# Kernel optimization log

Hardware: AMD Instinct MI355X
Metric: run time of the kernel (lower is better)

The kernel has to match this reference:

```python
import jax, jax.numpy as jnp
import numpy as np
import math

D_MODEL = 1024
N_HEADS = 16
D_HEAD = D_MODEL // N_HEADS
BIAS_HIDDEN = 32
B, N = 2, 1024


def setup_inputs() -> dict:
    key = jax.random.key(0)
    ks = jax.random.split(key, 16)
    s = 1.0 / math.sqrt(D_MODEL)
    inp = {
        "x": jax.random.normal(ks[0], (B, N, D_MODEL), dtype=jnp.float32),
        "xyz": jax.random.normal(ks[1], (B, N, 3), dtype=jnp.float32),
        "Wq": jax.random.normal(ks[2], (D_MODEL, D_MODEL), jnp.float32) * s,
        "bq": jnp.zeros((D_MODEL,), jnp.float32),
        "Wk": jax.random.normal(ks[3], (D_MODEL, D_MODEL), jnp.float32) * s,
        "bk": jnp.zeros((D_MODEL,), jnp.float32),
        "Wv": jax.random.normal(ks[4], (D_MODEL, D_MODEL), jnp.float32) * s,
        "bv": jnp.zeros((D_MODEL,), jnp.float32),
        "Wo": jax.random.normal(ks[5], (D_MODEL, D_MODEL), jnp.float32) * s,
        "bo": jnp.zeros((D_MODEL,), jnp.float32),
        "W1": jax.random.normal(ks[6], (3, BIAS_HIDDEN), jnp.float32) * (1.0 / math.sqrt(3.0)),
        "b1": jnp.zeros((BIAS_HIDDEN,), jnp.float32),
        "W2": jax.random.normal(ks[7], (BIAS_HIDDEN, N_HEADS), jnp.float32) * (1.0 / math.sqrt(BIAS_HIDDEN)),
        "b2": jnp.zeros((N_HEADS,), jnp.float32),
    }
    return inp


def reference(x, xyz, Wq, bq, Wk, bk, Wv, bv, Wo, bo, W1, b1, W2, b2):
    Bv, Nv, _ = x.shape
    # q,k,v projections -> [B, H, N, Dh]
    def proj(W, b):
        return (x @ W + b).reshape(Bv, Nv, N_HEADS, D_HEAD).transpose(0, 2, 1, 3)
    q = proj(Wq, bq)
    k = proj(Wk, bk)
    v = proj(Wv, bv)
    scores = jnp.einsum('bhid,bhjd->bhij', q, k) / math.sqrt(D_HEAD)
    # pairwise relative positions -> per-head bias via tiny MLP
    rel_pos = xyz[:, :, None, :] - xyz[:, None, :, :]            # [B,N,N,3]
    hidden = jax.nn.relu(rel_pos @ W1 + b1)                      # [B,N,N,hid]
    bias = (hidden @ W2 + b2).transpose(0, 3, 1, 2)              # [B,H,N,N]
    attn = jax.nn.softmax(scores + bias, axis=-1)                # [B,H,N,N]
    out = jnp.einsum('bhij,bhjd->bhid', attn, v)                 # [B,H,N,Dh]
    out = out.transpose(0, 2, 1, 3).reshape(Bv, Nv, D_MODEL)
    out = out @ Wo + bo
    return (out, attn)
```

## Files before the change

### kernel.cpp

```cpp
#include <hip/hip_runtime.h>
#include <hip/hip_bf16.h>
#include <math.h>

#define NTOK   1024
#define DMODEL 1024
#define NHEADS 16
#define DHEAD  64

typedef __attribute__((ext_vector_type(8))) short short8;
typedef __attribute__((ext_vector_type(4))) float floatx4;
#define MFMA(a,b,c) __builtin_amdgcn_mfma_f32_16x16x32_bf16(a,b,c,0,0,0)

__device__ __forceinline__ void bf16_split(float f, ushort& h, ushort& l) {
    unsigned u = __float_as_uint(f);
    unsigned hr = (u + 0x7FFFu + ((u >> 16) & 1u)) >> 16;
    h = (ushort)hr;
    float fh = __uint_as_float(hr << 16);
    float res = f - fh;
    unsigned u2 = __float_as_uint(res);
    l = (ushort)((u2 + 0x7FFFu + ((u2 >> 16) & 1u)) >> 16);
}

__global__ __launch_bounds__(256) void bias_kernel(
    const float* __restrict__ xyz,
    const float* __restrict__ W1, const float* __restrict__ b1,
    const float* __restrict__ W2, const float* __restrict__ b2,
    float* __restrict__ attnO)
{
    __shared__ float wbuf[656];
    int tid = threadIdx.x;
    for (int i = tid; i < 656; i += 256) {
        float v;
        if (i < 96)       v = W1[i];
        else if (i < 128) v = b1[i - 96];
        else if (i < 640) v = W2[i - 128];
        else              v = b2[i - 640];
        wbuf[i] = v;
    }
    __syncthreads();
    const float* w1s = wbuf;
    const float* b1s = wbuf + 96;
    const float* w2s = wbuf + 128;
    const float* b2s = wbuf + 640;

    int j = blockIdx.x * 256 + tid;
    int i = blockIdx.y;
    int b = blockIdx.z;

    float xi0 = xyz[((size_t)b * NTOK + i) * 3 + 0];
    float xi1 = xyz[((size_t)b * NTOK + i) * 3 + 1];
    float xi2 = xyz[((size_t)b * NTOK + i) * 3 + 2];
    float d0 = xi0 - xyz[((size_t)b * NTOK + j) * 3 + 0];
    float d1 = xi1 - xyz[((size_t)b * NTOK + j) * 3 + 1];
    float d2 = xi2 - xyz[((size_t)b * NTOK + j) * 3 + 2];

    float h[32];
#pragma unroll
    for (int hh = 0; hh < 32; ++hh) {
        float v = b1s[hh] + d0 * w1s[hh] + d1 * w1s[32 + hh] + d2 * w1s[64 + hh];
        h[hh] = fmaxf(v, 0.f);
    }
    size_t base = (size_t)b * NHEADS * 1048576 + (size_t)i * 1024 + j;
#pragma unroll
    for (int hd = 0; hd < NHEADS; ++hd) {
        float acc = b2s[hd];
#pragma unroll
        for (int hh = 0; hh < 32; ++hh) acc += h[hh] * w2s[hh * 16 + hd];
        attnO[base + (size_t)hd * 1048576] = acc;
    }
}

__global__ __launch_bounds__(256) void convx_kernel(
    const float* __restrict__ x, ushort* __restrict__ xh, ushort* __restrict__ xl)
{
    int id = blockIdx.x * 256 + threadIdx.x;
    float4 v = ((const float4*)x)[id];
    ushort h0,h1,h2,h3,l0,l1,l2,l3;
    bf16_split(v.x,h0,l0); bf16_split(v.y,h1,l1);
    bf16_split(v.z,h2,l2); bf16_split(v.w,h3,l3);
    ushort4 hv; hv.x=h0; hv.y=h1; hv.z=h2; hv.w=h3;
    ushort4 lv; lv.x=l0; lv.y=l1; lv.z=l2; lv.w=l3;
    ((ushort4*)xh)[id] = hv;
    ((ushort4*)xl)[id] = lv;
}

__global__ __launch_bounds__(256) void convw_kernel(
    const float* __restrict__ Wq, const float* __restrict__ Wk,
    const float* __restrict__ Wv, const float* __restrict__ Wo,
    ushort* __restrict__ Wcth, ushort* __restrict__ Wctl,
    ushort* __restrict__ Woth, ushort* __restrict__ Wotl)
{
    __shared__ float t[64][65];
    int z = blockIdx.z;
    const float* W = (z == 0) ? Wq : (z == 1) ? Wk : (z == 2) ? Wv : Wo;
    int n0 = blockIdx.x * 64, k0 = blockIdx.y * 64;
    int tid = threadIdx.x;
    int c4 = tid & 15, rr = tid >> 4;
#pragma unroll
    for (int t4 = 0; t4 < 4; ++t4) {
        int row = rr + t4 * 16;
        float4 v = *(const float4*)&W[(size_t)(k0 + row) * 1024 + n0 + c4 * 4];
        t[row][c4 * 4 + 0] = v.x; t[row][c4 * 4 + 1] = v.y;
        t[row][c4 * 4 + 2] = v.z; t[row][c4 * 4 + 3] = v.w;
    }
    __syncthreads();
    ushort* oh = (z < 3) ? Wcth : Woth;
    ushort* ol = (z < 3) ? Wctl : Wotl;
    int nbase = (z < 3) ? z * 1024 : 0;
#pragma unroll
    for (int t4 = 0; t4 < 4; ++t4) {
        int nl = rr + t4 * 16;
        int kk = c4 * 4;
        ushort4 hv, lv;
        ushort h, l;
        bf16_split(t[kk + 0][nl], h, l); hv.x = h; lv.x = l;
        bf16_split(t[kk + 1][nl], h, l); hv.y = h; lv.y = l;
        bf16_split(t[kk + 2][nl], h, l); hv.z = h; lv.z = l;
        bf16_split(t[kk + 3][nl], h, l); hv.w = h; lv.w = l;
        size_t o = (size_t)(nbase + n0 + nl) * 1024 + k0 + kk;
        *(ushort4*)&oh[o] = hv;
        *(ushort4*)&ol[o] = lv;
    }
}

__global__ __launch_bounds__(256) void mm_kernel(
    const ushort* __restrict__ Ah, const ushort* __restrict__ Al,
    const ushort* __restrict__ Bh, const ushort* __restrict__ Bl,
    const float* __restrict__ bq, const float* __restrict__ bk,
    const float* __restrict__ bv,
    float* __restrict__ out,
    ushort* __restrict__ qh, ushort* __restrict__ ql,
    ushort* __restrict__ kh, ushort* __restrict__ kl,
    ushort* __restrict__ vth, ushort* __restrict__ vtl,
    int mode)
{
    int n0 = blockIdx.x * 64;
    int m0 = blockIdx.y * 128;
    int w = threadIdx.x >> 6, l = threadIdx.x & 63;
    int li = l & 15, lg = l >> 4;
    int mrow = m0 + w * 32;

    const ushort* a0h = Ah + (size_t)(mrow + li) * 1024;
    const ushort* a0l = Al + (size_t)(mrow + li) * 1024;
    const ushort* a1h = Ah + (size_t)(mrow + 16 + li) * 1024;
    const ushort* a1l = Al + (size_t)(mrow + 16 + li) * 1024;
    const ushort* b0h = Bh + (size_t)(n0 +  0 + li) * 1024;
    const ushort* b1h = Bh + (size_t)(n0 + 16 + li) * 1024;
    const ushort* b2h = Bh + (size_t)(n0 + 32 + li) * 1024;
    const ushort* b3h = Bh + (size_t)(n0 + 48 + li) * 1024;
    const ushort* b0l = Bl + (size_t)(n0 +  0 + li) * 1024;
    const ushort* b1l = Bl + (size_t)(n0 + 16 + li) * 1024;
    const ushort* b2l = Bl + (size_t)(n0 + 32 + li) * 1024;
    const ushort* b3l = Bl + (size_t)(n0 + 48 + li) * 1024;

    floatx4 acc[2][4];
#pragma unroll
    for (int i = 0; i < 2; ++i)
#pragma unroll
        for (int j = 0; j < 4; ++j) acc[i][j] = (floatx4){0.f, 0.f, 0.f, 0.f};

    for (int ks = 0; ks < 32; ++ks) {
        int ko = ks * 32 + lg * 8;
        short8 A0h = *(const short8*)(a0h + ko);
        short8 A0l = *(const short8*)(a0l + ko);
        short8 A1h = *(const short8*)(a1h + ko);
        short8 A1l = *(const short8*)(a1l + ko);
#pragma unroll
        for (int nf = 0; nf < 4; ++nf) {
            const ushort* bhp = (nf == 0) ? b0h : (nf == 1) ? b1h : (nf == 2) ? b2h : b3h;
            const ushort* blp = (nf == 0) ? b0l : (nf == 1) ? b1l : (nf == 2) ? b2l : b3l;
            short8 Bh8 = *(const short8*)(bhp + ko);
            short8 Bl8 = *(const short8*)(blp + ko);
            acc[0][nf] = MFMA(A0h, Bh8, acc[0][nf]);
            acc[0][nf] = MFMA(A0h, Bl8, acc[0][nf]);
            acc[0][nf] = MFMA(A0l, Bh8, acc[0][nf]);
            acc[1][nf] = MFMA(A1h, Bh8, acc[1][nf]);
            acc[1][nf] = MFMA(A1h, Bl8, acc[1][nf]);
            acc[1][nf] = MFMA(A1l, Bh8, acc[1][nf]);
        }
    }

    if (mode == 0) {
#pragma unroll
        for (int fm = 0; fm < 2; ++fm)
#pragma unroll
            for (int nf = 0; nf < 4; ++nf) {
                int col = n0 + nf * 16 + li;
                float bval = bq[col];
#pragma unroll
                for (int r = 0; r < 4; ++r) {
                    int row = mrow + fm * 16 + lg * 4 + r;
                    out[(size_t)row * 1024 + col] = acc[fm][nf][r] + bval;
                }
            }
    } else {
        int z = n0 >> 10;
        const float* bp = (z == 0) ? bq : (z == 1) ? bk : bv;
#pragma unroll
        for (int fm = 0; fm < 2; ++fm)
#pragma unroll
            for (int nf = 0; nf < 4; ++nf) {
                int col = n0 + nf * 16 + li;
                int nloc = col & 1023;
                int hd = nloc >> 6, d = nloc & 63;
                float bval = bp[nloc];
#pragma unroll
                for (int r = 0; r < 4; ++r) {
                    int row = mrow + fm * 16 + lg * 4 + r;
                    int b = row >> 10, nn = row & 1023;
                    int bh = b * NHEADS + hd;
                    float v = acc[fm][nf][r] + bval;
                    ushort h, lo; bf16_split(v, h, lo);
                    if (z == 0) {
                        size_t o = ((size_t)bh * NTOK + nn) * DHEAD + d;
                        qh[o] = h; ql[o] = lo;
                    } else if (z == 1) {
                        size_t o = ((size_t)bh * NTOK + nn) * DHEAD + d;
                        kh[o] = h; kl[o] = lo;
                    } else {
                        size_t o = ((size_t)bh * DHEAD + d) * NTOK + nn;
                        vth[o] = h; vtl[o] = lo;
                    }
                }
            }
    }
}

__global__ __launch_bounds__(256) void score_kernel(
    const ushort* __restrict__ qh, const ushort* __restrict__ ql,
    const ushort* __restrict__ kh, const ushort* __restrict__ kl,
    float* __restrict__ attnO)
{
    __shared__ float redM[4][16];
    __shared__ float redS[4][16];
    int qt = blockIdx.x, hd = blockIdx.y, b = blockIdx.z;
    int bh = b * NHEADS + hd;
    int w = threadIdx.x >> 6, l = threadIdx.x & 63;
    int li = l & 15, lg = l >> 4;

    size_t qoff = ((size_t)bh * NTOK + qt * 16 + li) * DHEAD + lg * 8;
    short8 q0h = *(const short8*)(qh + qoff);
    short8 q0l = *(const short8*)(ql + qoff);
    short8 q1h = *(const short8*)(qh + qoff + 32);
    short8 q1l = *(const short8*)(ql + qoff + 32);

    floatx4 acc[16];
#pragma unroll
    for (int jf = 0; jf < 16; ++jf) acc[jf] = (floatx4){0.f, 0.f, 0.f, 0.f};

    int jbase = w * 256;
#pragma unroll
    for (int jf = 0; jf < 16; ++jf) {
        size_t koff = ((size_t)bh * NTOK + jbase + jf * 16 + li) * DHEAD + lg * 8;
        short8 K0h = *(const short8*)(kh + koff);
        short8 K0l = *(const short8*)(kl + koff);
        short8 K1h = *(const short8*)(kh + koff + 32);
        short8 K1l = *(const short8*)(kl + koff + 32);
        acc[jf] = MFMA(q0h, K0h, acc[jf]);
        acc[jf] = MFMA(q0h, K0l, acc[jf]);
        acc[jf] = MFMA(q0l, K0h, acc[jf]);
        acc[jf] = MFMA(q1h, K1h, acc[jf]);
        acc[jf] = MFMA(q1h, K1l, acc[jf]);
        acc[jf] = MFMA(q1l, K1h, acc[jf]);
    }

    float* prow = attnO + ((size_t)bh * NTOK + qt * 16) * NTOK;

    float mloc[4] = {-1e30f, -1e30f, -1e30f, -1e30f};
#pragma unroll
    for (int jf = 0; jf < 16; ++jf)
#pragma unroll
        for (int r = 0; r < 4; ++r) {
            float s = acc[jf][r] * 0.125f
                    + prow[(size_t)(lg * 4 + r) * NTOK + jbase + jf * 16 + li];
            acc[jf][r] = s;
            mloc[r] = fmaxf(mloc[r], s);
        }
#pragma unroll
    for (int r = 0; r < 4; ++r) {
        float m = mloc[r];
        m = fmaxf(m, __shfl_xor(m, 1, 64));
        m = fmaxf(m, __shfl_xor(m, 2, 64));
        m = fmaxf(m, __shfl_xor(m, 4, 64));
        m = fmaxf(m, __shfl_xor(m, 8, 64));
        mloc[r] = m;
    }
    if (li == 0) {
#pragma unroll
        for (int r = 0; r < 4; ++r) redM[w][lg * 4 + r] = mloc[r];
    }
    __syncthreads();
    float M[4];
#pragma unroll
    for (int r = 0; r < 4; ++r) {
        int row = lg * 4 + r;
        M[r] = fmaxf(fmaxf(redM[0][row], redM[1][row]),
                     fmaxf(redM[2][row], redM[3][row]));
    }
    float sloc[4] = {0.f, 0.f, 0.f, 0.f};
#pragma unroll
    for (int jf = 0; jf < 16; ++jf)
#pragma unroll
        for (int r = 0; r < 4; ++r) {
            float e = __expf(acc[jf][r] - M[r]);
            acc[jf][r] = e;
            sloc[r] += e;
        }
#pragma unroll
    for (int r = 0; r < 4; ++r) {
        float s = sloc[r];
        s += __shfl_xor(s, 1, 64);
        s += __shfl_xor(s, 2, 64);
        s += __shfl_xor(s, 4, 64);
        s += __shfl_xor(s, 8, 64);
        sloc[r] = s;
    }
    if (li == 0) {
#pragma unroll
        for (int r = 0; r < 4; ++r) redS[w][lg * 4 + r] = sloc[r];
    }
    __syncthreads();
    float inv[4];
#pragma unroll
    for (int r = 0; r < 4; ++r) {
        int row = lg * 4 + r;
        inv[r] = 1.0f / (redS[0][row] + redS[1][row] + redS[2][row] + redS[3][row]);
    }
#pragma unroll
    for (int jf = 0; jf < 16; ++jf)
#pragma unroll
        for (int r = 0; r < 4; ++r)
            prow[(size_t)(lg * 4 + r) * NTOK + jbase + jf * 16 + li] = acc[jf][r] * inv[r];
}

__global__ __launch_bounds__(256) void pv_kernel(
    const float* __restrict__ attnP,
    const ushort* __restrict__ vth, const ushort* __restrict__ vtl,
    ushort* __restrict__ awh, ushort* __restrict__ awl)
{
    int mt = blockIdx.x;
    int bh = blockIdx.y;
    int b = bh >> 4, hd = bh & 15;
    int w = threadIdx.x >> 6, l = threadIdx.x & 63;
    int li = l & 15, lg = l >> 4;
    int mrow = mt * 128 + w * 32;

    const float* P0 = attnP + ((size_t)bh * NTOK + mrow + li) * NTOK;
    const float* P1 = attnP + ((size_t)bh * NTOK + mrow + 16 + li) * NTOK;
    const ushort* v0h = vth + ((size_t)bh * DHEAD +  0 + li) * NTOK;
    const ushort* v1h = vth + ((size_t)bh * DHEAD + 16 + li) * NTOK;
    const ushort* v2h = vth + ((size_t)bh * DHEAD + 32 + li) * NTOK;
    const ushort* v3h = vth + ((size_t)bh * DHEAD + 48 + li) * NTOK;
    const ushort* v0l = vtl + ((size_t)bh * DHEAD +  0 + li) * NTOK;
    const ushort* v1l = vtl + ((size_t)bh * DHEAD + 16 + li) * NTOK;
    const ushort* v2l = vtl + ((size_t)bh * DHEAD + 32 + li) * NTOK;
    const ushort* v3l = vtl + ((size_t)bh * DHEAD + 48 + li) * NTOK;

    floatx4 acc[2][4];
#pragma unroll
    for (int i = 0; i < 2; ++i)
#pragma unroll
        for (int j = 0; j < 4; ++j) acc[i][j] = (floatx4){0.f, 0.f, 0.f, 0.f};

    for (int ks = 0; ks < 32; ++ks) {
        int ko = ks * 32 + lg * 8;
        float pa[8], pb[8];
        {
            float4 t0 = *(const float4*)(P0 + ko);
            float4 t1 = *(const float4*)(P0 + ko + 4);
            pa[0]=t0.x; pa[1]=t0.y; pa[2]=t0.z; pa[3]=t0.w;
            pa[4]=t1.x; pa[5]=t1.y; pa[6]=t1.z; pa[7]=t1.w;
            float4 t2 = *(const float4*)(P1 + ko);
            float4 t3 = *(const float4*)(P1 + ko + 4);
            pb[0]=t2.x; pb[1]=t2.y; pb[2]=t2.z; pb[3]=t2.w;
            pb[4]=t3.x; pb[5]=t3.y; pb[6]=t3.z; pb[7]=t3.w;
        }
        short8 A0h, A0l, A1h, A1l;
#pragma unroll
        for (int e = 0; e < 8; ++e) {
            ushort h, lo;
            bf16_split(pa[e], h, lo); A0h[e] = (short)h; A0l[e] = (short)lo;
            bf16_split(pb[e], h, lo); A1h[e] = (short)h; A1l[e] = (short)lo;
        }
#pragma unroll
        for (int nf = 0; nf < 4; ++nf) {
            const ushort* vhp = (nf == 0) ? v0h : (nf == 1) ? v1h : (nf == 2) ? v2h : v3h;
            const ushort* vlp = (nf == 0) ? v0l : (nf == 1) ? v1l : (nf == 2) ? v2l : v3l;
            short8 Bh8 = *(const short8*)(vhp + ko);
            short8 Bl8 = *(const short8*)(vlp + ko);
            acc[0][nf] = MFMA(A0h, Bh8, acc[0][nf]);
            acc[0][nf] = MFMA(A0h, Bl8, acc[0][nf]);
            acc[0][nf] = MFMA(A0l, Bh8, acc[0][nf]);
            acc[1][nf] = MFMA(A1h, Bh8, acc[1][nf]);
            acc[1][nf] = MFMA(A1h, Bl8, acc[1][nf]);
            acc[1][nf] = MFMA(A1l, Bh8, acc[1][nf]);
        }
    }
#pragma unroll
    for (int fm = 0; fm < 2; ++fm)
#pragma unroll
        for (int nf = 0; nf < 4; ++nf)
#pragma unroll
            for (int r = 0; r < 4; ++r) {
                int token = mrow + fm * 16 + lg * 4 + r;
                int d = nf * 16 + li;
                float v = acc[fm][nf][r];
                ushort h, lo; bf16_split(v, h, lo);
                size_t o = ((size_t)(b * NTOK + token)) * DMODEL + hd * DHEAD + d;
                awh[o] = h; awl[o] = lo;
            }
}

extern "C" void kernel_launch(void* const* d_in, const int* in_sizes, int n_in,
                              void* d_out, int out_size, void* d_ws, size_t ws_size,
                              hipStream_t stream)
{
    const float* x   = (const float*)d_in[0];
    const float* xyz = (const float*)d_in[1];
    const float* Wq  = (const float*)d_in[2];
    const float* bq  = (const float*)d_in[3];
    const float* Wk  = (const float*)d_in[4];
    const float* bk  = (const float*)d_in[5];
    const float* Wv  = (const float*)d_in[6];
    const float* bv  = (const float*)d_in[7];
    const float* Wo  = (const float*)d_in[8];
    const float* bo  = (const float*)d_in[9];
    const float* W1  = (const float*)d_in[10];
    const float* b1  = (const float*)d_in[11];
    const float* W2  = (const float*)d_in[12];
    const float* b2  = (const float*)d_in[13];

    const size_t OUT_ELEMS = (size_t)2 * NTOK * DMODEL;
    float* out   = (float*)d_out;
    float* attnO = out + OUT_ELEMS;

    char* ws = (char*)d_ws;
    ushort* Wcth = (ushort*)(ws);
    ushort* Wctl = (ushort*)(ws + 6291456);
    ushort* Woth = (ushort*)(ws + 12582912);
    ushort* Wotl = (ushort*)(ws + 14680064);
    ushort* qh   = (ushort*)(ws + 16777216);
    ushort* ql   = (ushort*)(ws + 20971520);
    ushort* kh   = (ushort*)(ws + 25165824);
    ushort* kl   = (ushort*)(ws + 29360128);
    ushort* vth  = (ushort*)(ws + 33554432);
    ushort* vtl  = (ushort*)(ws + 37748736);
    ushort* xh   = (ushort*)(ws + 41943040);
    ushort* xl   = (ushort*)(ws + 46137344);
    ushort* awh  = xh;
    ushort* awl  = xl;

    bias_kernel<<<dim3(4, 1024, 2), 256, 0, stream>>>(xyz, W1, b1, W2, b2, attnO);
    convx_kernel<<<dim3(2048), 256, 0, stream>>>(x, xh, xl);
    convw_kernel<<<dim3(16, 16, 4), 256, 0, stream>>>(Wq, Wk, Wv, Wo,
                                                      Wcth, Wctl, Woth, Wotl);
    mm_kernel<<<dim3(48, 16), 256, 0, stream>>>(xh, xl, Wcth, Wctl,
                                                bq, bk, bv, nullptr,
                                                qh, ql, kh, kl, vth, vtl, 1);
    score_kernel<<<dim3(64, NHEADS, 2), 256, 0, stream>>>(qh, ql, kh, kl, attnO);
    pv_kernel<<<dim3(8, 32), 256, 0, stream>>>(attnO, vth, vtl, awh, awl);
    mm_kernel<<<dim3(16, 16), 256, 0, stream>>>(awh, awl, Woth, Wotl,
                                                bo, bo, bo, out,
                                                nullptr, nullptr, nullptr, nullptr,
                                                nullptr, nullptr, 0);
}
```

Baseline: 529.6 us.

## Stage GEMM operand tiles in swizzled LDS via direct global-to-LDS loads

The split-bf16 GEMM kernel now stages 64x64 tiles of A-high, A-low, B-high and B-low into shared memory, each wave loading one operand with global_load_lds. The tile uses an XOR swizzle to avoid LDS bank conflicts. Waves then read MFMA fragments from LDS in a 2x2 wave layout instead of every wave streaming its own rows from global memory. The M tile shrinks from 128 to 64 to fit, which doubles the grid. This is meant to cut redundant global/L2 traffic in the QKV and output projections, at the cost of two barriers per k-step and no double buffering.

```diff
diff --git a/kernel.cpp b/kernel.cpp
--- a/kernel.cpp
+++ b/kernel.cpp
@@ -20,6 +20,8 @@
     unsigned u2 = __float_as_uint(res);
     l = (ushort)((u2 + 0x7FFFu + ((u2 >> 16) & 1u)) >> 16);
 }
+
+__device__ __forceinline__ int swzK(int r) { return (r & 7) ^ ((r >> 3) & 7); }
 
 __global__ __launch_bounds__(256) void bias_kernel(
     const float* __restrict__ xyz,
@@ -134,63 +136,79 @@
     ushort* __restrict__ vth, ushort* __restrict__ vtl,
     int mode)
 {
+    __shared__ ushort lds[4][64][64];
+
     int n0 = blockIdx.x * 64;
-    int m0 = blockIdx.y * 128;
+    int m0 = blockIdx.y * 64;
     int w = threadIdx.x >> 6, l = threadIdx.x & 63;
     int li = l & 15, lg = l >> 4;
-    int mrow = m0 + w * 32;
-
-    const ushort* a0h = Ah + (size_t)(mrow + li) * 1024;
-    const ushort* a0l = Al + (size_t)(mrow + li) * 1024;
-    const ushort* a1h = Ah + (size_t)(mrow + 16 + li) * 1024;
-    const ushort* a1l = Al + (size_t)(mrow + 16 + li) * 1024;
-    const ushort* b0h = Bh + (size_t)(n0 +  0 + li) * 1024;
-    const ushort* b1h = Bh + (size_t)(n0 + 16 + li) * 1024;
-    const ushort* b2h = Bh + (size_t)(n0 + 32 + li) * 1024;
-    const ushort* b3h = Bh + (size_t)(n0 + 48 + li) * 1024;
-    const ushort* b0l = Bl + (size_t)(n0 +  0 + li) * 1024;
-    const ushort* b1l = Bl + (size_t)(n0 + 16 + li) * 1024;
-    const ushort* b2l = Bl + (size_t)(n0 + 32 + li) * 1024;
-    const ushort* b3l = Bl + (size_t)(n0 + 48 + li) * 1024;
-
-    floatx4 acc[2][4];
+    int wm = w >> 1, wn = w & 1;
+
+    const ushort* gbase;
+    if      (w == 0) gbase = Ah + (size_t)m0 * 1024;
+    else if (w == 1) gbase = Al + (size_t)m0 * 1024;
+    else if (w == 2) gbase = Bh + (size_t)n0 * 1024;
+    else             gbase = Bl + (size_t)n0 * 1024;
+    ushort* lbase = &lds[w][0][0];
+    int srow = l >> 3;
+    int sc   = l & 7;
+
+    floatx4 acc[2][2];
 #pragma unroll
     for (int i = 0; i < 2; ++i)
 #pragma unroll
-        for (int j = 0; j < 4; ++j) acc[i][j] = (floatx4){0.f, 0.f, 0.f, 0.f};
-
-    for (int ks = 0; ks < 32; ++ks) {
-        int ko = ks * 32 + lg * 8;
-        short8 A0h = *(const short8*)(a0h + ko);
-        short8 A0l = *(const short8*)(a0l + ko);
-        short8 A1h = *(const short8*)(a1h + ko);
-        short8 A1l = *(const short8*)(a1l + ko);
-#pragma unroll
-        for (int nf = 0; nf < 4; ++nf) {
-            const ushort* bhp = (nf == 0) ? b0h : (nf == 1) ? b1h : (nf == 2) ? b2h : b3h;
-            const ushort* blp = (nf == 0) ? b0l : (nf == 1) ? b1l : (nf == 2) ? b2l : b3l;
-            short8 Bh8 = *(const short8*)(bhp + ko);
-            short8 Bl8 = *(const short8*)(blp + ko);
-            acc[0][nf] = MFMA(A0h, Bh8, acc[0][nf]);
-            acc[0][nf] = MFMA(A0h, Bl8, acc[0][nf]);
-            acc[0][nf] = MFMA(A0l, Bh8, acc[0][nf]);
-            acc[1][nf] = MFMA(A1h, Bh8, acc[1][nf]);
-            acc[1][nf] = MFMA(A1h, Bl8, acc[1][nf]);
-            acc[1][nf] = MFMA(A1l, Bh8, acc[1][nf]);
-        }
+        for (int j = 0; j < 2; ++j) acc[i][j] = (floatx4){0.f, 0.f, 0.f, 0.f};
+
+    for (int ks = 0; ks < 16; ++ks) {
+        int k0 = ks * 64;
+#pragma unroll
+        for (int t = 0; t < 8; ++t) {
+            int rl = t * 8 + srow;
+            int cs = sc ^ swzK(rl);
+            const ushort* g = gbase + (size_t)rl * 1024 + k0 + cs * 8;
+            __builtin_amdgcn_global_load_lds(
+                (const __attribute__((address_space(1))) unsigned int*)g,
+                (__attribute__((address_space(3))) unsigned int*)(lbase + t * 512),
+                16, 0, 0);
+        }
+        __syncthreads();
+#pragma unroll
+        for (int kk = 0; kk < 2; ++kk) {
+            short8 a[2][2], b2[2][2];
+#pragma unroll
+            for (int f = 0; f < 2; ++f) {
+                int ra = wm * 32 + f * 16 + li;
+                int ca = ((kk * 4 + lg) ^ swzK(ra)) * 8;
+                a[f][0] = *(const short8*)&lds[0][ra][ca];
+                a[f][1] = *(const short8*)&lds[1][ra][ca];
+                int rb = wn * 32 + f * 16 + li;
+                int cb = ((kk * 4 + lg) ^ swzK(rb)) * 8;
+                b2[f][0] = *(const short8*)&lds[2][rb][cb];
+                b2[f][1] = *(const short8*)&lds[3][rb][cb];
+            }
+#pragma unroll
+            for (int fm = 0; fm < 2; ++fm)
+#pragma unroll
+                for (int fn = 0; fn < 2; ++fn) {
+                    acc[fm][fn] = MFMA(a[fm][0], b2[fn][0], acc[fm][fn]);
+                    acc[fm][fn] = MFMA(a[fm][0], b2[fn][1], acc[fm][fn]);
+                    acc[fm][fn] = MFMA(a[fm][1], b2[fn][0], acc[fm][fn]);
+                }
+        }
+        __syncthreads();
     }
 
     if (mode == 0) {
 #pragma unroll
         for (int fm = 0; fm < 2; ++fm)
 #pragma unroll
-            for (int nf = 0; nf < 4; ++nf) {
-                int col = n0 + nf * 16 + li;
+            for (int fn = 0; fn < 2; ++fn) {
+                int col = n0 + wn * 32 + fn * 16 + li;
                 float bval = bq[col];
 #pragma unroll
                 for (int r = 0; r < 4; ++r) {
-                    int row = mrow + fm * 16 + lg * 4 + r;
-                    out[(size_t)row * 1024 + col] = acc[fm][nf][r] + bval;
+                    int row = m0 + wm * 32 + fm * 16 + lg * 4 + r;
+                    out[(size_t)row * 1024 + col] = acc[fm][fn][r] + bval;
                 }
             }
     } else {
@@ -199,17 +217,17 @@
 #pragma unroll
         for (int fm = 0; fm < 2; ++fm)
 #pragma unroll
-            for (int nf = 0; nf < 4; ++nf) {
-                int col = n0 + nf * 16 + li;
+            for (int fn = 0; fn < 2; ++fn) {
+                int col = n0 + wn * 32 + fn * 16 + li;
                 int nloc = col & 1023;
                 int hd = nloc >> 6, d = nloc & 63;
                 float bval = bp[nloc];
 #pragma unroll
                 for (int r = 0; r < 4; ++r) {
-                    int row = mrow + fm * 16 + lg * 4 + r;
+                    int row = m0 + wm * 32 + fm * 16 + lg * 4 + r;
                     int b = row >> 10, nn = row & 1023;
                     int bh = b * NHEADS + hd;
-                    float v = acc[fm][nf][r] + bval;
+                    float v = acc[fm][fn][r] + bval;
                     ushort h, lo; bf16_split(v, h, lo);
                     if (z == 0) {
                         size_t o = ((size_t)bh * NTOK + nn) * DHEAD + d;
@@ -454,12 +472,12 @@
     convx_kernel<<<dim3(2048), 256, 0, stream>>>(x, xh, xl);
     convw_kernel<<<dim3(16, 16, 4), 256, 0, stream>>>(Wq, Wk, Wv, Wo,
                                                       Wcth, Wctl, Woth, Wotl);
-    mm_kernel<<<dim3(48, 16), 256, 0, stream>>>(xh, xl, Wcth, Wctl,
+    mm_kernel<<<dim3(48, 32), 256, 0, stream>>>(xh, xl, Wcth, Wctl,
                                                 bq, bk, bv, nullptr,
                                                 qh, ql, kh, kl, vth, vtl, 1);
     score_kernel<<<dim3(64, NHEADS, 2), 256, 0, stream>>>(qh, ql, kh, kl, attnO);
     pv_kernel<<<dim3(8, 32), 256, 0, stream>>>(attnO, vth, vtl, awh, awl);
-    mm_kernel<<<dim3(16, 16), 256, 0, stream>>>(awh, awl, Woth, Wotl,
+    mm_kernel<<<dim3(16, 32), 256, 0, stream>>>(awh, awl, Woth, Wotl,
                                                 bo, bo, bo, out,
                                                 nullptr, nullptr, nullptr, nullptr,
                                                 nullptr, nullptr, 0);
```

Measured after the change: 427.8 us. 1.24x faster.
